# Kernel optimization log

Hardware: AMD Instinct MI355X
Metric: run time of the kernel (lower is better)

## Reference

```python
import jax, jax.numpy as jnp
import numpy as np

B, S, D, H = 256, 196, 2048, 512  # batch, att_size, rnn_size, att_hid_size


def setup_inputs() -> dict:
    key = jax.random.key(0)
    ks = jax.random.split(key, 5)
    return {
        "h": jax.random.normal(ks[0], (B, D), jnp.float32),
        "att_feats": jax.random.normal(ks[1], (B, S, D), jnp.float32),
        "p_att_feats": jax.random.normal(ks[2], (B, S, H), jnp.float32),
        "att_masks": jnp.ones((B, S), jnp.float32),
        "W_h2att": jax.random.normal(ks[3], (H, D), jnp.float32) * (1.0 / np.sqrt(D)),
        "b_h2att": jnp.zeros((H,), jnp.float32),
        "w_alpha": jax.random.normal(ks[4], (H,), jnp.float32) * (1.0 / np.sqrt(H)),
        "b_alpha": jnp.zeros((), jnp.float32),
    }


def reference(h, att_feats, p_att_feats, att_masks, W_h2att, b_h2att, w_alpha, b_alpha):
    # h2att: [B, D] -> [B, H]
    att_h = jnp.einsum("bd,hd->bh", h, W_h2att) + b_h2att
    # broadcast add + tanh: [B, S, H]
    dot = jnp.tanh(p_att_feats + att_h[:, None, :])
    # alpha_net: reduce hidden dim to a scalar score per slot -> [B, S]
    scores = jnp.einsum("bsh,h->bs", dot, w_alpha) + b_alpha
    weight = jax.nn.softmax(scores, axis=1)
    # masked renormalization (att_masks provided)
    weight = weight * att_masks
    weight = weight / jnp.sum(weight, axis=1, keepdims=True)
    # weighted sum of att_feats: [B, D]
    att_res = jnp.einsum("bs,bsd->bd", weight, att_feats)
    return att_res
```

## Files before the change

kernel.cpp:

```cpp
#include <hip/hip_runtime.h>
#include <hip/hip_bf16.h>
#include <math.h>


#define B_ 256
#define S_ 196
#define D_ 2048
#define H_ 512

__device__ __forceinline__ float fast_tanh(float x) {
  float e = __expf(2.0f * x);
  return 1.0f - 2.0f * __builtin_amdgcn_rcpf(e + 1.0f);
}

__global__ __launch_bounds__(256) void h2att_kernel(
    const float* __restrict__ h, const float* __restrict__ W,
    const float* __restrict__ bias, float* __restrict__ att_h) {
  __shared__ float lds_a[32][33];
  __shared__ float lds_b[32][33];

  const int tid = threadIdx.x;
  const int m0 = blockIdx.y * 32;
  const int n0 = blockIdx.x * 32;

  const int lr = tid >> 3;
  const int lc = (tid & 7) * 4;
  const int tm = tid >> 4;
  const int tn = tid & 15;

  float acc00 = 0.f, acc01 = 0.f, acc10 = 0.f, acc11 = 0.f;

  for (int k0 = 0; k0 < D_; k0 += 32) {
    float4 av = *(const float4*)(h + (size_t)(m0 + lr) * D_ + k0 + lc);
    float4 bv = *(const float4*)(W + (size_t)(n0 + lr) * D_ + k0 + lc);
    __syncthreads();
    lds_a[lr][lc + 0] = av.x; lds_a[lr][lc + 1] = av.y;
    lds_a[lr][lc + 2] = av.z; lds_a[lr][lc + 3] = av.w;
    lds_b[lr][lc + 0] = bv.x; lds_b[lr][lc + 1] = bv.y;
    lds_b[lr][lc + 2] = bv.z; lds_b[lr][lc + 3] = bv.w;
    __syncthreads();
#pragma unroll
    for (int kk = 0; kk < 32; ++kk) {
      float a0 = lds_a[tm][kk];
      float a1 = lds_a[tm + 16][kk];
      float b0 = lds_b[tn][kk];
      float b1 = lds_b[tn + 16][kk];
      acc00 = fmaf(a0, b0, acc00);
      acc01 = fmaf(a0, b1, acc01);
      acc10 = fmaf(a1, b0, acc10);
      acc11 = fmaf(a1, b1, acc11);
    }
  }

  const int m = m0 + tm, n = n0 + tn;
  float bn0 = bias[n], bn1 = bias[n + 16];
  att_h[(size_t)m * H_ + n]              = acc00 + bn0;
  att_h[(size_t)m * H_ + n + 16]         = acc01 + bn1;
  att_h[(size_t)(m + 16) * H_ + n]       = acc10 + bn0;
  att_h[(size_t)(m + 16) * H_ + n + 16]  = acc11 + bn1;
}

__global__ __launch_bounds__(256) void scores_kernel(
    const float* __restrict__ p, const float* __restrict__ att_h,
    const float* __restrict__ w_alpha, const float* __restrict__ b_alpha,
    float* __restrict__ scores) {
  const int wave = threadIdx.x >> 6;
  const int lane = threadIdx.x & 63;
  const int idx = blockIdx.x * 4 + wave;
  const int b = idx / S_;

  const float* pp = p + (size_t)idx * H_;
  const float* ah = att_h + (size_t)b * H_;

  float acc = 0.f;
#pragma unroll
  for (int h0 = 0; h0 < H_; h0 += 256) {
    const int o = h0 + lane * 4;
    float4 pv = *(const float4*)(pp + o);
    float4 av = *(const float4*)(ah + o);
    float4 wv = *(const float4*)(w_alpha + o);
    acc += fast_tanh(pv.x + av.x) * wv.x;
    acc += fast_tanh(pv.y + av.y) * wv.y;
    acc += fast_tanh(pv.z + av.z) * wv.z;
    acc += fast_tanh(pv.w + av.w) * wv.w;
  }
#pragma unroll
  for (int off = 32; off > 0; off >>= 1) acc += __shfl_down(acc, off);
  if (lane == 0) scores[idx] = acc + b_alpha[0];
}

__global__ __launch_bounds__(256) void softmax_kernel(
    const float* __restrict__ scores, const float* __restrict__ mask,
    float* __restrict__ weight) {
  __shared__ float red[4];
  const int tid = threadIdx.x;
  const int b = blockIdx.x;
  const int wave = tid >> 6, lane = tid & 63;

  float sc = (tid < S_) ? scores[(size_t)b * S_ + tid] : -INFINITY;

  float v = sc;
#pragma unroll
  for (int off = 32; off > 0; off >>= 1) v = fmaxf(v, __shfl_down(v, off));
  if (lane == 0) red[wave] = v;
  __syncthreads();
  float mx = fmaxf(fmaxf(red[0], red[1]), fmaxf(red[2], red[3]));
  __syncthreads();

  float e = (tid < S_) ? __expf(sc - mx) : 0.f;

  v = e;
#pragma unroll
  for (int off = 32; off > 0; off >>= 1) v += __shfl_down(v, off);
  if (lane == 0) red[wave] = v;
  __syncthreads();
  float z = red[0] + red[1] + red[2] + red[3];
  __syncthreads();

  float w = (tid < S_) ? (e / z) * mask[(size_t)b * S_ + tid] : 0.f;

  v = w;
#pragma unroll
  for (int off = 32; off > 0; off >>= 1) v += __shfl_down(v, off);
  if (lane == 0) red[wave] = v;
  __syncthreads();
  float z2 = red[0] + red[1] + red[2] + red[3];

  if (tid < S_) weight[(size_t)b * S_ + tid] = w / z2;
}

__global__ __launch_bounds__(128) void attres_kernel(
    const float* __restrict__ weight, const float* __restrict__ att_feats,
    float* __restrict__ out) {
  __shared__ float w_lds[S_];
  const int tid = threadIdx.x;
  const int b = blockIdx.y;

  if (tid < S_) w_lds[tid] = weight[(size_t)b * S_ + tid];
  if (tid + 128 < S_) w_lds[tid + 128] = weight[(size_t)b * S_ + tid + 128];
  __syncthreads();

  const int d0 = blockIdx.x * 512 + tid * 4;
  const float* base = att_feats + (size_t)b * S_ * D_ + d0;

  float4 acc = {0.f, 0.f, 0.f, 0.f};
#pragma unroll 2
  for (int so = 0; so < S_; so += 7) {
    float4 v0 = *(const float4*)(base + (size_t)(so + 0) * D_);
    float4 v1 = *(const float4*)(base + (size_t)(so + 1) * D_);
    float4 v2 = *(const float4*)(base + (size_t)(so + 2) * D_);
    float4 v3 = *(const float4*)(base + (size_t)(so + 3) * D_);
    float4 v4 = *(const float4*)(base + (size_t)(so + 4) * D_);
    float4 v5 = *(const float4*)(base + (size_t)(so + 5) * D_);
    float4 v6 = *(const float4*)(base + (size_t)(so + 6) * D_);
    float w0 = w_lds[so + 0], w1 = w_lds[so + 1], w2 = w_lds[so + 2];
    float w3 = w_lds[so + 3], w4 = w_lds[so + 4], w5 = w_lds[so + 5];
    float w6 = w_lds[so + 6];
    acc.x = fmaf(w0, v0.x, acc.x); acc.y = fmaf(w0, v0.y, acc.y);
    acc.z = fmaf(w0, v0.z, acc.z); acc.w = fmaf(w0, v0.w, acc.w);
    acc.x = fmaf(w1, v1.x, acc.x); acc.y = fmaf(w1, v1.y, acc.y);
    acc.z = fmaf(w1, v1.z, acc.z); acc.w = fmaf(w1, v1.w, acc.w);
    acc.x = fmaf(w2, v2.x, acc.x); acc.y = fmaf(w2, v2.y, acc.y);
    acc.z = fmaf(w2, v2.z, acc.z); acc.w = fmaf(w2, v2.w, acc.w);
    acc.x = fmaf(w3, v3.x, acc.x); acc.y = fmaf(w3, v3.y, acc.y);
    acc.z = fmaf(w3, v3.z, acc.z); acc.w = fmaf(w3, v3.w, acc.w);
    acc.x = fmaf(w4, v4.x, acc.x); acc.y = fmaf(w4, v4.y, acc.y);
    acc.z = fmaf(w4, v4.z, acc.z); acc.w = fmaf(w4, v4.w, acc.w);
    acc.x = fmaf(w5, v5.x, acc.x); acc.y = fmaf(w5, v5.y, acc.y);
    acc.z = fmaf(w5, v5.z, acc.z); acc.w = fmaf(w5, v5.w, acc.w);
    acc.x = fmaf(w6, v6.x, acc.x); acc.y = fmaf(w6, v6.y, acc.y);
    acc.z = fmaf(w6, v6.z, acc.z); acc.w = fmaf(w6, v6.w, acc.w);
  }
  *(float4*)(out + (size_t)b * D_ + d0) = acc;
}

extern "C" void kernel_launch(void* const* d_in, const int* in_sizes, int n_in,
                              void* d_out, int out_size, void* d_ws, size_t ws_size,
                              hipStream_t stream) {
  const float* h         = (const float*)d_in[0];
  const float* att_feats = (const float*)d_in[1];
  const float* p_att     = (const float*)d_in[2];
  const float* att_masks = (const float*)d_in[3];
  const float* W_h2att   = (const float*)d_in[4];
  const float* b_h2att   = (const float*)d_in[5];
  const float* w_alpha   = (const float*)d_in[6];
  const float* b_alpha   = (const float*)d_in[7];
  float* out = (float*)d_out;

  float* att_h  = (float*)d_ws;
  float* scores = att_h + (size_t)B_ * H_;
  float* weight = scores + (size_t)B_ * S_;

  dim3 g1(H_ / 32, B_ / 32);
  h2att_kernel<<<g1, 256, 0, stream>>>(h, W_h2att, b_h2att, att_h);

  scores_kernel<<<(B_ * S_) / 4, 256, 0, stream>>>(p_att, att_h, w_alpha,
                                                   b_alpha, scores);

  softmax_kernel<<<B_, 256, 0, stream>>>(scores, att_masks, weight);

  dim3 g4(D_ / 512, B_);
  attres_kernel<<<g4, 128, 0, stream>>>(weight, att_feats, out);
}
```

Before: 679.4 us.

## Split-K h2att GEMM with 64x64 register tiles and atomic accumulation

The h2att GEMM moves from 32x32 tiles with 2x2 per-thread outputs to 64x64 tiles with 4x4 per-thread outputs. The K dimension is split into 16 slices across grid z, and partial sums are combined with atomicAdd into att_h. A separate kernel preloads att_h with the bias first. The aim is more parallelism (512 blocks instead of 128) and more reuse per LDS read. In exchange it adds an extra launch and atomic traffic, and the float summation order is no longer deterministic.

```diff
diff --git a/kernel.cpp b/kernel.cpp
--- a/kernel.cpp
+++ b/kernel.cpp
@@ -13,51 +13,68 @@
   return 1.0f - 2.0f * __builtin_amdgcn_rcpf(e + 1.0f);
 }
 
+__global__ __launch_bounds__(256) void bias_init_kernel(
+    const float* __restrict__ bias, float* __restrict__ att_h) {
+  const int idx = blockIdx.x * 256 + threadIdx.x;
+  const int n4 = (idx * 4) & (H_ - 1);
+  float4 bv = *(const float4*)(bias + n4);
+  *(float4*)(att_h + (size_t)idx * 4) = bv;
+}
+
 __global__ __launch_bounds__(256) void h2att_kernel(
     const float* __restrict__ h, const float* __restrict__ W,
-    const float* __restrict__ bias, float* __restrict__ att_h) {
-  __shared__ float lds_a[32][33];
-  __shared__ float lds_b[32][33];
+    float* __restrict__ att_h) {
+#define LSTR 68
+  __shared__ float a_lds[32][LSTR];
+  __shared__ float b_lds[32][LSTR];
 
   const int tid = threadIdx.x;
-  const int m0 = blockIdx.y * 32;
-  const int n0 = blockIdx.x * 32;
-
-  const int lr = tid >> 3;
-  const int lc = (tid & 7) * 4;
-  const int tm = tid >> 4;
-  const int tn = tid & 15;
-
-  float acc00 = 0.f, acc01 = 0.f, acc10 = 0.f, acc11 = 0.f;
-
-  for (int k0 = 0; k0 < D_; k0 += 32) {
-    float4 av = *(const float4*)(h + (size_t)(m0 + lr) * D_ + k0 + lc);
-    float4 bv = *(const float4*)(W + (size_t)(n0 + lr) * D_ + k0 + lc);
+  const int n0 = blockIdx.x * 64;
+  const int m0 = blockIdx.y * 64;
+  const int kslice = blockIdx.z * 128;
+
+  const int sr = tid >> 2;
+  const int sk = (tid & 3) * 8;
+  const int tm = (tid >> 4) * 4;
+  const int tn = (tid & 15) * 4;
+
+  float acc[4][4] = {};
+
+  for (int k0 = 0; k0 < 128; k0 += 32) {
+    const size_t ka = (size_t)kslice + k0 + sk;
+    float4 a0 = *(const float4*)(h + (size_t)(m0 + sr) * D_ + ka);
+    float4 a1 = *(const float4*)(h + (size_t)(m0 + sr) * D_ + ka + 4);
+    float4 b0 = *(const float4*)(W + (size_t)(n0 + sr) * D_ + ka);
+    float4 b1 = *(const float4*)(W + (size_t)(n0 + sr) * D_ + ka + 4);
     __syncthreads();
-    lds_a[lr][lc + 0] = av.x; lds_a[lr][lc + 1] = av.y;
-    lds_a[lr][lc + 2] = av.z; lds_a[lr][lc + 3] = av.w;
-    lds_b[lr][lc + 0] = bv.x; lds_b[lr][lc + 1] = bv.y;
-    lds_b[lr][lc + 2] = bv.z; lds_b[lr][lc + 3] = bv.w;
+    a_lds[sk + 0][sr] = a0.x; a_lds[sk + 1][sr] = a0.y;
+    a_lds[sk + 2][sr] = a0.z; a_lds[sk + 3][sr] = a0.w;
+    a_lds[sk + 4][sr] = a1.x; a_lds[sk + 5][sr] = a1.y;
+    a_lds[sk + 6][sr] = a1.z; a_lds[sk + 7][sr] = a1.w;
+    b_lds[sk + 0][sr] = b0.x; b_lds[sk + 1][sr] = b0.y;
+    b_lds[sk + 2][sr] = b0.z; b_lds[sk + 3][sr] = b0.w;
+    b_lds[sk + 4][sr] = b1.x; b_lds[sk + 5][sr] = b1.y;
+    b_lds[sk + 6][sr] = b1.z; b_lds[sk + 7][sr] = b1.w;
     __syncthreads();
 #pragma unroll
     for (int kk = 0; kk < 32; ++kk) {
-      float a0 = lds_a[tm][kk];
-      float a1 = lds_a[tm + 16][kk];
-      float b0 = lds_b[tn][kk];
-      float b1 = lds_b[tn + 16][kk];
-      acc00 = fmaf(a0, b0, acc00);
-      acc01 = fmaf(a0, b1, acc01);
-      acc10 = fmaf(a1, b0, acc10);
-      acc11 = fmaf(a1, b1, acc11);
+      float4 av = *(const float4*)(&a_lds[kk][tm]);
+      float4 bv = *(const float4*)(&b_lds[kk][tn]);
+      float a[4] = {av.x, av.y, av.z, av.w};
+      float b[4] = {bv.x, bv.y, bv.z, bv.w};
+#pragma unroll
+      for (int i = 0; i < 4; ++i)
+#pragma unroll
+        for (int j = 0; j < 4; ++j) acc[i][j] = fmaf(a[i], b[j], acc[i][j]);
     }
   }
 
-  const int m = m0 + tm, n = n0 + tn;
-  float bn0 = bias[n], bn1 = bias[n + 16];
-  att_h[(size_t)m * H_ + n]              = acc00 + bn0;
-  att_h[(size_t)m * H_ + n + 16]         = acc01 + bn1;
-  att_h[(size_t)(m + 16) * H_ + n]       = acc10 + bn0;
-  att_h[(size_t)(m + 16) * H_ + n + 16]  = acc11 + bn1;
+#pragma unroll
+  for (int i = 0; i < 4; ++i)
+#pragma unroll
+    for (int j = 0; j < 4; ++j)
+      atomicAdd(att_h + (size_t)(m0 + tm + i) * H_ + n0 + tn + j, acc[i][j]);
+#undef LSTR
 }
 
 __global__ __launch_bounds__(256) void scores_kernel(
@@ -191,8 +208,10 @@
   float* scores = att_h + (size_t)B_ * H_;
   float* weight = scores + (size_t)B_ * S_;
 
-  dim3 g1(H_ / 32, B_ / 32);
-  h2att_kernel<<<g1, 256, 0, stream>>>(h, W_h2att, b_h2att, att_h);
+  bias_init_kernel<<<128, 256, 0, stream>>>(b_h2att, att_h);
+
+  dim3 g1(H_ / 64, B_ / 64, 16);
+  h2att_kernel<<<g1, 256, 0, stream>>>(h, W_h2att, att_h);
 
   scores_kernel<<<(B_ * S_) / 4, 256, 0, stream>>>(p_att, att_h, w_alpha,
                                                    b_alpha, scores);
```

Result: faster. 638.4 us (-6.0%).
